# Performance work log

Hardware: AMD Instinct MI355X
Metric: run time of the kernel (lower is better)

The kernel has to match this reference:

```python
import jax, jax.numpy as jnp
import numpy as np

DIM = 1024
HEADS = 16
DIM_HEAD = DIM // HEADS  # 64
B, N = 4, 1024


def setup_inputs() -> dict:
    key = jax.random.key(0)
    ks = jax.random.split(key, 8)
    s = 1.0 / np.sqrt(DIM)
    inp = {
        "x": jax.random.normal(ks[0], (B, N, DIM), dtype=jnp.float32),
        # weights stored as [in, out] so y = x @ W (+ b), equivalent to torch Linear
        "Wq": jax.random.normal(ks[1], (DIM, DIM), dtype=jnp.float32) * s,
        "Wk": jax.random.normal(ks[2], (DIM, DIM), dtype=jnp.float32) * s,
        "Wv": jax.random.normal(ks[3], (DIM, DIM), dtype=jnp.float32) * s,
        "Wproj": jax.random.normal(ks[4], (DIM, DIM), dtype=jnp.float32) * s,
        "bproj": jnp.zeros((DIM,), dtype=jnp.float32),
        "Wpre": jax.random.normal(ks[5], (DIM, DIM), dtype=jnp.float32) * s,
        "bpre": jnp.zeros((DIM,), dtype=jnp.float32),
        # original init is -inf (non-runnable); use a finite trained value
        "pi": jnp.full((1,), 0.5, dtype=jnp.float32),
    }
    return inp


def reference(x, Wq, Wk, Wv, Wproj, bproj, Wpre, bpre, pi):
    b, n, c = x.shape
    h, dh = HEADS, DIM_HEAD
    residual = x
    # bias-logit path: Linear -> SiLU -> bmm with itself (dropout p=0 is identity)
    pre = jax.nn.silu(x @ Wpre + bpre)                       # [B,N,C]
    logits = jnp.einsum('bnc,bmc->bnm', pre, pre) / jnp.sqrt(jnp.float32(c))
    # QKV (x2 defaults to x)
    q = (x @ Wq).reshape(b, n, h, dh).transpose(0, 2, 1, 3)  # [B,H,N,Dh]
    k = (x @ Wk).reshape(b, n, h, dh).transpose(0, 2, 1, 3)
    v = (x @ Wv).reshape(b, n, h, dh).transpose(0, 2, 1, 3)
    score = jnp.einsum('bhnd,bhmd->bhnm', q, k) / jnp.sqrt(jnp.float32(dh))
    final_logits = pi[0] * logits[:, None, :, :] + score     # broadcast bias over heads
    attn = jax.nn.softmax(final_logits, axis=-1)
    out = jnp.einsum('bhnm,bhmd->bhnd', attn, v)             # [B,H,N,Dh]
    out = out.transpose(0, 2, 1, 3).reshape(b, n, h * dh)
    out = out @ Wproj + bproj
    return out + residual
```

## Files before the change

kernel.cpp:

```cpp
#include <hip/hip_runtime.h>

using bf16x8 = __attribute__((ext_vector_type(8))) short;
using v8bf   = __attribute__((ext_vector_type(8))) __bf16;
using f32x4  = __attribute__((ext_vector_type(4))) float;
using u32x2  = __attribute__((ext_vector_type(2))) unsigned;
using bf16x2 = __attribute__((ext_vector_type(2))) __bf16;

typedef const __attribute__((address_space(1))) void GASV;
typedef __attribute__((address_space(3))) void LASV;

template <typename V>
__device__ __forceinline__ auto mfma_bf16_impl(V a, V b, f32x4 c, int)
    -> decltype(__builtin_amdgcn_mfma_f32_16x16x32_bf16(a, b, c, 0, 0, 0)) {
  return __builtin_amdgcn_mfma_f32_16x16x32_bf16(a, b, c, 0, 0, 0);
}
template <typename V>
__device__ __forceinline__ f32x4 mfma_bf16_impl(V a, V b, f32x4 c, long) {
  return __builtin_amdgcn_mfma_f32_16x16x32_bf16(
      __builtin_bit_cast(v8bf, a), __builtin_bit_cast(v8bf, b), c, 0, 0, 0);
}
__device__ __forceinline__ f32x4 MFMA(bf16x8 a, bf16x8 b, f32x4 c) {
  return mfma_bf16_impl(a, b, c, 0);
}

__device__ __forceinline__ void async_lds16(const void* g, void* l) {
  __builtin_amdgcn_global_load_lds((GASV*)g, (LASV*)l, 16, 0, 0);
}

__device__ __forceinline__ unsigned short f2bf(float x) {
  unsigned u = __float_as_uint(x);
  u = u + 0x7fffu + ((u >> 16) & 1u);
  return (unsigned short)(u >> 16);
}

__device__ __forceinline__ unsigned pack_bf2(float lo, float hi) {
  bf16x2 t;
  t[0] = (__bf16)lo;
  t[1] = (__bf16)hi;
  return __builtin_bit_cast(unsigned, t);
}

#define LOG2E 1.4426950408889634f
#define SOFT_OFF 14.0f

__global__ __launch_bounds__(256) void k_prep(
    const float4* __restrict__ x, ushort4* __restrict__ xb,
    const float* __restrict__ w0, const float* __restrict__ w1,
    const float* __restrict__ w2, const float* __restrict__ w3,
    const float* __restrict__ w4, unsigned short* __restrict__ out) {
  const int bid = blockIdx.x, tid = threadIdx.x;
  if (bid < 4096) {
    const int i = bid * 256 + tid;
    float4 v = x[i];
    ushort4 p;
    p.x = f2bf(v.x); p.y = f2bf(v.y); p.z = f2bf(v.z); p.w = f2bf(v.w);
    xb[i] = p;
    return;
  }
  __shared__ float t[32][33];
  const int tb = bid - 4096;
  const int z = tb >> 10;
  const float* W = (z == 0) ? w0 : (z == 1) ? w1 : (z == 2) ? w2 : (z == 3) ? w3 : w4;
  const float sc = (z == 1) ? (LOG2E / 8.0f) : 1.0f;
  unsigned short* o = out + (size_t)z * (1u << 20);
  const int bx = (tb & 31) * 32, by = ((tb >> 5) & 31) * 32;
  const int tx = tid & 31, ty = tid >> 5;
#pragma unroll
  for (int i = 0; i < 4; ++i)
    t[ty + i * 8][tx] = W[(size_t)(by + ty + i * 8) * 1024 + bx + tx];
  __syncthreads();
#pragma unroll
  for (int i = 0; i < 4; ++i)
    o[(size_t)(bx + ty + i * 8) * 1024 + by + tx] = f2bf(t[tx][ty + i * 8] * sc);
}

template <int MI, int NI>
__device__ __forceinline__ void gemm_core_t(const unsigned short* __restrict__ A,
                                            const unsigned short* __restrict__ Bt,
                                            unsigned short* ldsA,
                                            unsigned short* ldsB,
                                            f32x4 acc[MI][NI]) {
  const int tid = threadIdx.x;
  const int w = tid >> 6, lane = tid & 63;
  const int lane15 = lane & 15, quad = lane >> 4;
  const int wm = w >> 1, wn = w & 1;
  for (int ko = 0; ko < 16; ++ko) {
    __syncthreads();
#pragma unroll
    for (int i = 0; i < MI; ++i) {
      const int p = i * 256 + tid;
      const int r = p >> 3, cc = (p & 7) ^ (r & 7);
      async_lds16(A + r * 1024 + ko * 64 + cc * 8, ldsA + (i * 256 + w * 64) * 8);
    }
#pragma unroll
    for (int i = 0; i < NI; ++i) {
      const int p = i * 256 + tid;
      const int r = p >> 3, cc = (p & 7) ^ (r & 7);
      async_lds16(Bt + r * 1024 + ko * 64 + cc * 8, ldsB + (i * 256 + w * 64) * 8);
    }
    __syncthreads();
    bf16x8 af[MI][2], bfr[NI][2];
#pragma unroll
    for (int t = 0; t < MI; ++t) {
      const int row = wm * (MI * 16) + t * 16 + lane15;
#pragma unroll
      for (int h = 0; h < 2; ++h)
        af[t][h] = *(const bf16x8*)&ldsA[row * 64 + (((h * 4 + quad) ^ (row & 7)) << 3)];
    }
#pragma unroll
    for (int t = 0; t < NI; ++t) {
      const int row = wn * (NI * 16) + t * 16 + lane15;
#pragma unroll
      for (int h = 0; h < 2; ++h)
        bfr[t][h] = *(const bf16x8*)&ldsB[row * 64 + (((h * 4 + quad) ^ (row & 7)) << 3)];
    }
#pragma unroll
    for (int mi = 0; mi < MI; ++mi)
#pragma unroll
      for (int ni = 0; ni < NI; ++ni) {
        acc[mi][ni] = MFMA(af[mi][0], bfr[ni][0], acc[mi][ni]);
        acc[mi][ni] = MFMA(af[mi][1], bfr[ni][1], acc[mi][ni]);
      }
  }
}

#define GEMM_PROLOGUE(MI_, NI_)                                      \
  __shared__ unsigned short ldsA[(MI_)*32 * 64];                     \
  __shared__ unsigned short ldsB[(NI_)*32 * 64];                     \
  f32x4 acc[MI_][NI_];                                               \
  {                                                                  \
    f32x4 z_ = {0.f, 0.f, 0.f, 0.f};                                 \
    for (int i_ = 0; i_ < (MI_); ++i_)                               \
      for (int j_ = 0; j_ < (NI_); ++j_) acc[i_][j_] = z_;           \
  }

#define GEMM_EPI_IDX(MI_, NI_)                                       \
  const int tid = threadIdx.x, w = tid >> 6, lane = tid & 63;        \
  const int lane15 = lane & 15, quad = lane >> 4;                    \
  const int wm = w >> 1, wn = w & 1;                                 \
  const int r0 = tm + wm * ((MI_)*16) + quad * 4;                    \
  const int c0 = tn + wn * ((NI_)*16) + lane15;

__global__ __launch_bounds__(512, 4) void k_gemm_qkvpre(
    const unsigned short* __restrict__ xb, const unsigned short* __restrict__ wt,
    const float* __restrict__ bpre, unsigned short* __restrict__ pre,
    unsigned short* __restrict__ qb, unsigned short* __restrict__ kb,
    unsigned short* __restrict__ vt) {
  __shared__ unsigned short ldsA[2][256 * 32];
  __shared__ unsigned short ldsB[2][128 * 32];
  const int bid = blockIdx.x;
  const int xcd = bid & 7, idx = bid >> 3;
  const int z = xcd >> 1, half = xcd & 1;
  int tm, tn;
  if (z == 3) {
    tm = half * 2048 + (idx >> 3) * 256;
    tn = (idx & 7) * 128;
  } else {
    tm = (idx >> 4) * 256;
    tn = half * 2048 + (idx & 15) * 128;
  }
  const unsigned short* At =
      (z == 3) ? xb + (size_t)tm * 1024
               : wt + (size_t)z * (1u << 20) + (size_t)tm * 1024;
  const unsigned short* Bt_ =
      (z == 3) ? wt + (size_t)3 * (1u << 20) + (size_t)tn * 1024
               : xb + (size_t)tn * 1024;

  const int tid = threadIdx.x, w = tid >> 6, lane = tid & 63;
  const int lane15 = lane & 15, quad = lane >> 4;
  const int wm = w >> 1, wn = w & 1;

  f32x4 acc[4][4];
  {
    f32x4 z_ = {0.f, 0.f, 0.f, 0.f};
#pragma unroll
    for (int i = 0; i < 4; ++i)
#pragma unroll
      for (int j = 0; j < 4; ++j) acc[i][j] = z_;
  }

  auto stage = [&](int ko, int buf) {
#pragma unroll
    for (int j = 0; j < 2; ++j) {
      const int p = j * 512 + tid;
      const int r = p >> 2, cc = (p & 3) ^ ((r >> 1) & 3);
      async_lds16(At + (size_t)r * 1024 + ko * 32 + cc * 8,
                  &ldsA[buf][(j * 512 + w * 64) * 8]);
    }
    {
      const int p = tid;
      const int r = p >> 2, cc = (p & 3) ^ ((r >> 1) & 3);
      async_lds16(Bt_ + (size_t)r * 1024 + ko * 32 + cc * 8,
                  &ldsB[buf][(w * 64) * 8]);
    }
  };

  stage(0, 0);
  __syncthreads();
  for (int t = 0; t < 32; ++t) {
    const int buf = t & 1;
    if (t + 1 < 32) stage(t + 1, buf ^ 1);
    const unsigned short* sA = ldsA[buf];
    const unsigned short* sB = ldsB[buf];
    bf16x8 af[4], bf[4];
#pragma unroll
    for (int mi = 0; mi < 4; ++mi) {
      const int row = wm * 64 + mi * 16 + lane15;
      af[mi] = *(const bf16x8*)&sA[row * 32 + ((quad ^ ((row >> 1) & 3)) << 3)];
    }
#pragma unroll
    for (int ni = 0; ni < 4; ++ni) {
      const int row = wn * 64 + ni * 16 + lane15;
      bf[ni] = *(const bf16x8*)&sB[row * 32 + ((quad ^ ((row >> 1) & 3)) << 3)];
    }
    __builtin_amdgcn_s_setprio(1);
#pragma unroll
    for (int mi = 0; mi < 4; ++mi)
#pragma unroll
      for (int ni = 0; ni < 4; ++ni)
        acc[mi][ni] = MFMA(af[mi], bf[ni], acc[mi][ni]);
    __builtin_amdgcn_s_setprio(0);
    __syncthreads();
  }

  const int r0 = tm + wm * 64 + quad * 4;
  const int c0 = tn + wn * 64 + lane15;
  if (z == 0) {
#pragma unroll
    for (int mf = 0; mf < 4; ++mf) {
      const float4 b4 = *(const float4*)&bpre[r0 + mf * 16];
#pragma unroll
      for (int nf = 0; nf < 4; ++nf) {
        const int seq = c0 + nf * 16;
        float vv[4];
#pragma unroll
        for (int rr = 0; rr < 4; ++rr) {
          float v = acc[mf][nf][rr] + ((const float*)&b4)[rr];
          vv[rr] = v / (1.0f + __expf(-v));
        }
        ushort4 pk;
        pk.x = f2bf(vv[0]); pk.y = f2bf(vv[1]);
        pk.z = f2bf(vv[2]); pk.w = f2bf(vv[3]);
        *(ushort4*)&pre[(size_t)seq * 1024 + r0 + mf * 16] = pk;
      }
    }
  } else if (z == 1 || z == 2) {
    unsigned short* dst = (z == 1) ? qb : kb;
#pragma unroll
    for (int mf = 0; mf < 4; ++mf)
#pragma unroll
      for (int nf = 0; nf < 4; ++nf) {
        const int seq = c0 + nf * 16;
        ushort4 pk;
        pk.x = f2bf(acc[mf][nf][0]); pk.y = f2bf(acc[mf][nf][1]);
        pk.z = f2bf(acc[mf][nf][2]); pk.w = f2bf(acc[mf][nf][3]);
        *(ushort4*)&dst[(size_t)seq * 1024 + r0 + mf * 16] = pk;
      }
  } else {
#pragma unroll
    for (int mf = 0; mf < 4; ++mf) {
      const int m = r0 + mf * 16;
      const int bb_ = m >> 10, nseq = m & 1023;
#pragma unroll
      for (int nf = 0; nf < 4; ++nf) {
        const int cg = c0 + nf * 16;
        const int hh = cg >> 6, dd = cg & 63;
        ushort4 pk;
        pk.x = f2bf(acc[mf][nf][0]); pk.y = f2bf(acc[mf][nf][1]);
        pk.z = f2bf(acc[mf][nf][2]); pk.w = f2bf(acc[mf][nf][3]);
        *(ushort4*)&vt[(size_t)(((bb_ * 16 + hh) << 6) + dd) * 1024 + nseq] = pk;
      }
    }
  }
}

__global__ __launch_bounds__(256) void k_gemm_logits(
    const unsigned short* __restrict__ pre, const float* __restrict__ pi,
    unsigned short* __restrict__ lg) {
  const int bz = blockIdx.z;
  const unsigned short* base = pre + ((size_t)bz << 20);
  const int tm = blockIdx.y * 64, tn = blockIdx.x * 128;
  GEMM_PROLOGUE(2, 4);
  gemm_core_t<2, 4>(base + (size_t)tm * 1024, base + (size_t)tn * 1024, ldsA, ldsB, acc);
  const float sc = pi[0] * (LOG2E / 32.0f);
  GEMM_EPI_IDX(2, 4);
#pragma unroll
  for (int mi = 0; mi < 2; ++mi)
#pragma unroll
    for (int ni = 0; ni < 4; ++ni) {
      const int col = c0 + ni * 16;
      ushort4 pk;
      pk.x = f2bf(acc[mi][ni][0] * sc); pk.y = f2bf(acc[mi][ni][1] * sc);
      pk.z = f2bf(acc[mi][ni][2] * sc); pk.w = f2bf(acc[mi][ni][3] * sc);
      *(ushort4*)&lg[((size_t)bz << 20) + (size_t)col * 1024 + r0 + mi * 16] = pk;
    }
}

__global__ __launch_bounds__(256) void k_gemm_out(
    const unsigned short* __restrict__ ao, const unsigned short* __restrict__ wtp,
    const float* __restrict__ bproj, const float* __restrict__ xres,
    float* __restrict__ out) {
  const int tm = blockIdx.x * 64, tn = blockIdx.y * 128;
  GEMM_PROLOGUE(2, 4);
  gemm_core_t<2, 4>(wtp + (size_t)tm * 1024, ao + (size_t)tn * 1024, ldsA, ldsB, acc);
  GEMM_EPI_IDX(2, 4);
#pragma unroll
  for (int mi = 0; mi < 2; ++mi) {
    const float4 b4 = *(const float4*)&bproj[r0 + mi * 16];
#pragma unroll
    for (int ni = 0; ni < 4; ++ni) {
      const int seq = c0 + ni * 16;
      const size_t idx = (size_t)seq * 1024 + r0 + mi * 16;
      const float4 rv = *(const float4*)&xres[idx];
      float4 ov;
      ov.x = acc[mi][ni][0] + b4.x + rv.x;
      ov.y = acc[mi][ni][1] + b4.y + rv.y;
      ov.z = acc[mi][ni][2] + b4.z + rv.z;
      ov.w = acc[mi][ni][3] + b4.w + rv.w;
      *(float4*)&out[idx] = ov;
    }
  }
}

__global__ __launch_bounds__(256, 2) void k_attn(
    const unsigned short* __restrict__ qb, const unsigned short* __restrict__ kb,
    const unsigned short* __restrict__ vt, const unsigned short* __restrict__ lg,
    unsigned short* __restrict__ ao) {
  __shared__ unsigned short ldsK[2 * 64 * 64];
  __shared__ unsigned short ldsV[2 * 64 * 64];
  const int bid = blockIdx.x;
  const int xcd = bid & 7, idx = bid >> 3;
  const int b = xcd >> 1, hg = xcd & 1;
  const int h = hg * 8 + (idx >> 3);
  const int q0 = (idx & 7) * 128;
  const int tid = threadIdx.x, w = tid >> 6, lane = tid & 63;
  const int lane15 = lane & 15, quad = lane >> 4;
  const int qw = q0 + w * 32;

  bf16x8 qf[2][2];
#pragma unroll
  for (int qh = 0; qh < 2; ++qh) {
    const unsigned short* qrow =
        qb + (size_t)((b << 10) + qw + qh * 16 + lane15) * 1024 + (h << 6);
    qf[qh][0] = *(const bf16x8*)(qrow + quad * 8);
    qf[qh][1] = *(const bf16x8*)(qrow + 32 + quad * 8);
  }
  const unsigned short* kbase = kb + ((size_t)(b << 10)) * 1024 + (h << 6);
  const unsigned short* vbase = vt + ((size_t)((b * 16 + h) << 6)) * 1024;
  const unsigned short* lgrow =
      lg + ((size_t)b << 20) + (size_t)(qw + lane15) * 1024 +
      (quad >> 1) * 16 + (quad & 1) * 4;

  float lcol[2] = {0.f, 0.f};
  f32x4 o[2][4];
  {
    f32x4 z_ = {0.f, 0.f, 0.f, 0.f};
#pragma unroll
    for (int qh = 0; qh < 2; ++qh)
#pragma unroll
      for (int nt = 0; nt < 4; ++nt) o[qh][nt] = z_;
  }

  uint2 lgc[2][4], lgn[2][4];

  auto stage = [&](int ch, unsigned short* sK, unsigned short* sV) {
    const int kv0 = ch * 64;
#pragma unroll
    for (int i = 0; i < 2; ++i) {
      const int p = i * 256 + tid;
      const int r = p >> 3, cc = (p & 7) ^ (r & 7);
      const int rk = (r & 0x27) | ((r & 8) << 1) | ((r & 16) >> 1);
      async_lds16(kbase + (size_t)(kv0 + rk) * 1024 + cc * 8,
                  sK + (i * 256 + w * 64) * 8);
      async_lds16(vbase + (size_t)r * 1024 + kv0 + cc * 8,
                  sV + (i * 256 + w * 64) * 8);
    }
  };
  auto lgload = [&](int ch, uint2 dst[2][4]) {
#pragma unroll
    for (int qh = 0; qh < 2; ++qh)
#pragma unroll
      for (int mi = 0; mi < 4; ++mi)
        dst[qh][mi] = *(const uint2*)(lgrow + qh * 16 * 1024 + ch * 64 +
                                      (mi >> 1) * 32 + (mi & 1) * 8);
  };
  auto compute = [&](const unsigned short* sK, const unsigned short* sV) {
    f32x4 s[2][4];
    __builtin_amdgcn_s_setprio(1);
#pragma unroll
    for (int mi = 0; mi < 4; ++mi) {
      const int row = mi * 16 + lane15;
      bf16x8 k0 = *(const bf16x8*)&sK[row * 64 + ((quad ^ (row & 7)) << 3)];
      bf16x8 k1 = *(const bf16x8*)&sK[row * 64 + (((4 + quad) ^ (row & 7)) << 3)];
#pragma unroll
      for (int qh = 0; qh < 2; ++qh) {
        f32x4 t;
        t[0] = __uint_as_float(lgc[qh][mi].x << 16);
        t[1] = __uint_as_float(lgc[qh][mi].x & 0xffff0000u);
        t[2] = __uint_as_float(lgc[qh][mi].y << 16);
        t[3] = __uint_as_float(lgc[qh][mi].y & 0xffff0000u);
        t = MFMA(k0, qf[qh][0], t);
        t = MFMA(k1, qf[qh][1], t);
        s[qh][mi] = t;
      }
    }
    __builtin_amdgcn_s_setprio(0);
    uint2 pk[2][4];
#pragma unroll
    for (int qh = 0; qh < 2; ++qh) {
      float rs = 0.f;
#pragma unroll
      for (int mi = 0; mi < 4; ++mi) {
        const float p0 = __builtin_amdgcn_exp2f(s[qh][mi][0] - SOFT_OFF);
        const float p1 = __builtin_amdgcn_exp2f(s[qh][mi][1] - SOFT_OFF);
        const float p2 = __builtin_amdgcn_exp2f(s[qh][mi][2] - SOFT_OFF);
        const float p3 = __builtin_amdgcn_exp2f(s[qh][mi][3] - SOFT_OFF);
        rs += (p0 + p1) + (p2 + p3);
        pk[qh][mi].x = pack_bf2(p0, p1);
        pk[qh][mi].y = pack_bf2(p2, p3);
      }
      lcol[qh] += rs;
    }

#pragma unroll
    for (int kp = 0; kp < 2; ++kp) {
      bf16x8 vf[4];
#pragma unroll
      for (int dt = 0; dt < 4; ++dt) {
        const int d = dt * 16 + lane15;
        vf[dt] = *(const bf16x8*)&sV[d * 64 +
                                     (((kp * 4 + quad) ^ (d & 7)) << 3)];
      }
#pragma unroll
      for (int qh = 0; qh < 2; ++qh) {
        u32x2 rx = __builtin_amdgcn_permlane16_swap(pk[qh][2 * kp].x,
                                                    pk[qh][2 * kp + 1].x, 0, 0);
        u32x2 ry = __builtin_amdgcn_permlane16_swap(pk[qh][2 * kp].y,
                                                    pk[qh][2 * kp + 1].y, 0, 0);
        uint4 bfv;
        bfv.x = rx.x;
        bfv.y = ry.x;
        bfv.z = rx.y;
        bfv.w = ry.y;
        const bf16x8 pf = __builtin_bit_cast(bf16x8, bfv);
        __builtin_amdgcn_s_setprio(1);
#pragma unroll
        for (int dt = 0; dt < 4; ++dt)
          o[qh][dt] = MFMA(vf[dt], pf, o[qh][dt]);
        __builtin_amdgcn_s_setprio(0);
      }
    }
  };

  unsigned short* sK0 = ldsK;
  unsigned short* sK1 = ldsK + 64 * 64;
  unsigned short* sV0 = ldsV;
  unsigned short* sV1 = ldsV + 64 * 64;

  stage(0, sK0, sV0);
  lgload(0, lgc);
  __syncthreads();

  for (int c = 0; c < 16; c += 2) {
    stage(c + 1, sK1, sV1);
    lgload(c + 1, lgn);
    compute(sK0, sV0);
    __syncthreads();
#pragma unroll
    for (int qh = 0; qh < 2; ++qh)
#pragma unroll
      for (int mi = 0; mi < 4; ++mi) lgc[qh][mi] = lgn[qh][mi];
    if (c + 2 < 16) {
      stage(c + 2, sK0, sV0);
      lgload(c + 2, lgn);
    }
    compute(sK1, sV1);
    __syncthreads();
#pragma unroll
    for (int qh = 0; qh < 2; ++qh)
#pragma unroll
      for (int mi = 0; mi < 4; ++mi) lgc[qh][mi] = lgn[qh][mi];
  }

#pragma unroll
  for (int qh = 0; qh < 2; ++qh) {
    float lc = lcol[qh];
    lc += __shfl_xor(lc, 16);
    lc += __shfl_xor(lc, 32);
    const float rinv = 1.0f / lc;
    const int m = (b << 10) + qw + qh * 16 + lane15;
#pragma unroll
    for (int dt = 0; dt < 4; ++dt) {
      ushort4 pkk;
      pkk.x = f2bf(o[qh][dt][0] * rinv);
      pkk.y = f2bf(o[qh][dt][1] * rinv);
      pkk.z = f2bf(o[qh][dt][2] * rinv);
      pkk.w = f2bf(o[qh][dt][3] * rinv);
      *(ushort4*)&ao[(size_t)m * 1024 + (h << 6) + dt * 16 + quad * 4] = pkk;
    }
  }
}

extern "C" void kernel_launch(void* const* d_in, const int* in_sizes, int n_in,
                              void* d_out, int out_size, void* d_ws, size_t ws_size,
                              hipStream_t stream) {
  const float* x     = (const float*)d_in[0];
  const float* Wq    = (const float*)d_in[1];
  const float* Wk    = (const float*)d_in[2];
  const float* Wv    = (const float*)d_in[3];
  const float* Wproj = (const float*)d_in[4];
  const float* bproj = (const float*)d_in[5];
  const float* Wpre  = (const float*)d_in[6];
  const float* bpre  = (const float*)d_in[7];
  const float* pi    = (const float*)d_in[8];
  float* out = (float*)d_out;
  char* ws = (char*)d_ws;

  unsigned short* xb  = (unsigned short*)(ws);
  unsigned short* wt  = (unsigned short*)(ws + (8u << 20));
  unsigned short* pre = (unsigned short*)(ws + (18u << 20));
  unsigned short* qb  = (unsigned short*)(ws + (26u << 20));
  unsigned short* kb  = (unsigned short*)(ws + (34u << 20));
  unsigned short* vt  = (unsigned short*)(ws + (42u << 20));
  unsigned short* lg  = xb;
  unsigned short* ao  = pre;

  k_prep<<<dim3(4096 + 5120), dim3(256), 0, stream>>>(
      (const float4*)x, (ushort4*)xb, Wpre, Wq, Wk, Wv, Wproj, wt);
  k_gemm_qkvpre<<<dim3(512), dim3(512), 0, stream>>>(xb, wt, bpre, pre, qb, kb, vt);
  k_gemm_logits<<<dim3(8, 16, 4), dim3(256), 0, stream>>>(pre, pi, lg);
  k_attn<<<dim3(512), dim3(256), 0, stream>>>(qb, kb, vt, lg, ao);
  k_gemm_out<<<dim3(16, 32, 1), dim3(256), 0, stream>>>(ao, wt + 4 * (1u << 20), bproj, x, out);
}
```

Before: 209.2 us.

## Load A operand fragments directly from global into registers, staging only B in LDS

The QKV/pre GEMM kernel no longer stages the 256-row A tile through LDS. Each wave now loads its own A fragments straight from global memory into registers, double-buffered across iterations, and only the B tile goes through async LDS copies. This removes the A-side LDS traffic and halves LDS footprint, which could allow more resident blocks. In exchange, A rows are read from global by both column-waves (wn=0/1) without sharing, the 16-byte loads per lane are strided by rows, and extra registers are used for two fragment sets.

```diff
diff --git a/kernel.cpp b/kernel.cpp
--- a/kernel.cpp
+++ b/kernel.cpp
@@ -146,7 +146,6 @@
     const float* __restrict__ bpre, unsigned short* __restrict__ pre,
     unsigned short* __restrict__ qb, unsigned short* __restrict__ kb,
     unsigned short* __restrict__ vt) {
-  __shared__ unsigned short ldsA[2][256 * 32];
   __shared__ unsigned short ldsB[2][128 * 32];
   const int bid = blockIdx.x;
   const int xcd = bid & 7, idx = bid >> 3;
@@ -179,35 +178,19 @@
       for (int j = 0; j < 4; ++j) acc[i][j] = z_;
   }
 
-  auto stage = [&](int ko, int buf) {
-#pragma unroll
-    for (int j = 0; j < 2; ++j) {
-      const int p = j * 512 + tid;
-      const int r = p >> 2, cc = (p & 3) ^ ((r >> 1) & 3);
-      async_lds16(At + (size_t)r * 1024 + ko * 32 + cc * 8,
-                  &ldsA[buf][(j * 512 + w * 64) * 8]);
-    }
-    {
-      const int p = tid;
-      const int r = p >> 2, cc = (p & 3) ^ ((r >> 1) & 3);
-      async_lds16(Bt_ + (size_t)r * 1024 + ko * 32 + cc * 8,
-                  &ldsB[buf][(w * 64) * 8]);
-    }
+  auto stageB = [&](int ko, int buf) {
+    const int r = tid >> 2, cc = (tid & 3) ^ ((r >> 1) & 3);
+    async_lds16(Bt_ + (size_t)r * 1024 + ko * 32 + cc * 8,
+                &ldsB[buf][(w * 64) * 8]);
   };
-
-  stage(0, 0);
-  __syncthreads();
-  for (int t = 0; t < 32; ++t) {
-    const int buf = t & 1;
-    if (t + 1 < 32) stage(t + 1, buf ^ 1);
-    const unsigned short* sA = ldsA[buf];
-    const unsigned short* sB = ldsB[buf];
-    bf16x8 af[4], bf[4];
-#pragma unroll
-    for (int mi = 0; mi < 4; ++mi) {
-      const int row = wm * 64 + mi * 16 + lane15;
-      af[mi] = *(const bf16x8*)&sA[row * 32 + ((quad ^ ((row >> 1) & 3)) << 3)];
-    }
+  const unsigned short* arow = At + (size_t)(wm * 64 + lane15) * 1024 + quad * 8;
+  auto loadA = [&](bf16x8 af[4], int ko) {
+#pragma unroll
+    for (int mi = 0; mi < 4; ++mi)
+      af[mi] = *(const bf16x8*)(arow + (size_t)(mi * 16) * 1024 + ko * 32);
+  };
+  auto step = [&](const unsigned short* sB, const bf16x8 af[4]) {
+    bf16x8 bf[4];
 #pragma unroll
     for (int ni = 0; ni < 4; ++ni) {
       const int row = wn * 64 + ni * 16 + lane15;
@@ -220,6 +203,18 @@
       for (int ni = 0; ni < 4; ++ni)
         acc[mi][ni] = MFMA(af[mi], bf[ni], acc[mi][ni]);
     __builtin_amdgcn_s_setprio(0);
+  };
+
+  bf16x8 afA[4], afB[4];
+  stageB(0, 0);
+  loadA(afA, 0);
+  __syncthreads();
+  for (int t = 0; t < 32; t += 2) {
+    if (t + 1 < 32) { stageB(t + 1, 1); loadA(afB, t + 1); }
+    step(ldsB[0], afA);
+    __syncthreads();
+    if (t + 2 < 32) { stageB(t + 2, 0); loadA(afA, t + 2); }
+    step(ldsB[1], afB);
     __syncthreads();
   }
 
```

After: 247.9 us. 1.19x slower.

## Double-buffer LDS in logits and output-projection GEMMs with K=32 stages

Applied to the files above, without the earlier changes.

Replaces the single-buffered K=64 GEMM core used by the logits and output-projection kernels with a double-buffered core that prefetches the next K=32 slice into the alternate LDS buffer while MFMAs run on the current one. This leaves one barrier per iteration instead of two and raises wave priority around the MFMA block. The swizzle is adapted to 32-wide rows and launch bounds request two blocks per CU. In exchange the loop runs twice as many iterations, each with fewer MFMAs to hide the load latency.

```diff
diff --git a/kernel.cpp b/kernel.cpp
--- a/kernel.cpp
+++ b/kernel.cpp
@@ -74,72 +74,55 @@
     o[(size_t)(bx + ty + i * 8) * 1024 + by + tx] = f2bf(t[tx][ty + i * 8] * sc);
 }
 
-template <int MI, int NI>
-__device__ __forceinline__ void gemm_core_t(const unsigned short* __restrict__ A,
-                                            const unsigned short* __restrict__ Bt,
-                                            unsigned short* ldsA,
-                                            unsigned short* ldsB,
-                                            f32x4 acc[MI][NI]) {
-  const int tid = threadIdx.x;
-  const int w = tid >> 6, lane = tid & 63;
+__device__ __forceinline__ void gemm64x128_core(
+    const unsigned short* __restrict__ At, const unsigned short* __restrict__ Bt,
+    unsigned short (*ldsA)[64 * 32], unsigned short (*ldsB)[128 * 32],
+    f32x4 acc[2][4]) {
+  const int tid = threadIdx.x, w = tid >> 6, lane = tid & 63;
   const int lane15 = lane & 15, quad = lane >> 4;
   const int wm = w >> 1, wn = w & 1;
-  for (int ko = 0; ko < 16; ++ko) {
+  auto stage = [&](int ko, int buf) {
+    {
+      const int r = tid >> 2, cc = (tid & 3) ^ ((r >> 1) & 3);
+      async_lds16(At + (size_t)r * 1024 + ko * 32 + cc * 8,
+                  &ldsA[buf][(w * 64) * 8]);
+    }
+#pragma unroll
+    for (int j = 0; j < 2; ++j) {
+      const int p = j * 256 + tid;
+      const int r = p >> 2, cc = (p & 3) ^ ((r >> 1) & 3);
+      async_lds16(Bt + (size_t)r * 1024 + ko * 32 + cc * 8,
+                  &ldsB[buf][(j * 256 + w * 64) * 8]);
+    }
+  };
+  stage(0, 0);
+  __syncthreads();
+  for (int t = 0; t < 32; ++t) {
+    const int buf = t & 1;
+    if (t + 1 < 32) stage(t + 1, buf ^ 1);
+    const unsigned short* sA = ldsA[buf];
+    const unsigned short* sB = ldsB[buf];
+    bf16x8 af[2], bf[4];
+#pragma unroll
+    for (int mi = 0; mi < 2; ++mi) {
+      const int row = wm * 32 + mi * 16 + lane15;
+      af[mi] = *(const bf16x8*)&sA[row * 32 + ((quad ^ ((row >> 1) & 3)) << 3)];
+    }
+#pragma unroll
+    for (int ni = 0; ni < 4; ++ni) {
+      const int row = wn * 64 + ni * 16 + lane15;
+      bf[ni] = *(const bf16x8*)&sB[row * 32 + ((quad ^ ((row >> 1) & 3)) << 3)];
+    }
+    __builtin_amdgcn_s_setprio(1);
+#pragma unroll
+    for (int mi = 0; mi < 2; ++mi)
+#pragma unroll
+      for (int ni = 0; ni < 4; ++ni)
+        acc[mi][ni] = MFMA(af[mi], bf[ni], acc[mi][ni]);
+    __builtin_amdgcn_s_setprio(0);
     __syncthreads();
-#pragma unroll
-    for (int i = 0; i < MI; ++i) {
-      const int p = i * 256 + tid;
-      const int r = p >> 3, cc = (p & 7) ^ (r & 7);
-      async_lds16(A + r * 1024 + ko * 64 + cc * 8, ldsA + (i * 256 + w * 64) * 8);
-    }
-#pragma unroll
-    for (int i = 0; i < NI; ++i) {
-      const int p = i * 256 + tid;
-      const int r = p >> 3, cc = (p & 7) ^ (r & 7);
-      async_lds16(Bt + r * 1024 + ko * 64 + cc * 8, ldsB + (i * 256 + w * 64) * 8);
-    }
-    __syncthreads();
-    bf16x8 af[MI][2], bfr[NI][2];
-#pragma unroll
-    for (int t = 0; t < MI; ++t) {
-      const int row = wm * (MI * 16) + t * 16 + lane15;
-#pragma unroll
-      for (int h = 0; h < 2; ++h)
-        af[t][h] = *(const bf16x8*)&ldsA[row * 64 + (((h * 4 + quad) ^ (row & 7)) << 3)];
-    }
-#pragma unroll
-    for (int t = 0; t < NI; ++t) {
-      const int row = wn * (NI * 16) + t * 16 + lane15;
-#pragma unroll
-      for (int h = 0; h < 2; ++h)
-        bfr[t][h] = *(const bf16x8*)&ldsB[row * 64 + (((h * 4 + quad) ^ (row & 7)) << 3)];
-    }
-#pragma unroll
-    for (int mi = 0; mi < MI; ++mi)
-#pragma unroll
-      for (int ni = 0; ni < NI; ++ni) {
-        acc[mi][ni] = MFMA(af[mi][0], bfr[ni][0], acc[mi][ni]);
-        acc[mi][ni] = MFMA(af[mi][1], bfr[ni][1], acc[mi][ni]);
-      }
-  }
-}
-
-#define GEMM_PROLOGUE(MI_, NI_)                                      \
-  __shared__ unsigned short ldsA[(MI_)*32 * 64];                     \
-  __shared__ unsigned short ldsB[(NI_)*32 * 64];                     \
-  f32x4 acc[MI_][NI_];                                               \
-  {                                                                  \
-    f32x4 z_ = {0.f, 0.f, 0.f, 0.f};                                 \
-    for (int i_ = 0; i_ < (MI_); ++i_)                               \
-      for (int j_ = 0; j_ < (NI_); ++j_) acc[i_][j_] = z_;           \
-  }
-
-#define GEMM_EPI_IDX(MI_, NI_)                                       \
-  const int tid = threadIdx.x, w = tid >> 6, lane = tid & 63;        \
-  const int lane15 = lane & 15, quad = lane >> 4;                    \
-  const int wm = w >> 1, wn = w & 1;                                 \
-  const int r0 = tm + wm * ((MI_)*16) + quad * 4;                    \
-  const int c0 = tn + wn * ((NI_)*16) + lane15;
+  }
+}
 
 __global__ __launch_bounds__(512, 4) void k_gemm_qkvpre(
     const unsigned short* __restrict__ xb, const unsigned short* __restrict__ wt,
@@ -274,16 +257,30 @@
   }
 }
 
-__global__ __launch_bounds__(256) void k_gemm_logits(
+__global__ __launch_bounds__(256, 2) void k_gemm_logits(
     const unsigned short* __restrict__ pre, const float* __restrict__ pi,
     unsigned short* __restrict__ lg) {
+  __shared__ unsigned short ldsA[2][64 * 32];
+  __shared__ unsigned short ldsB[2][128 * 32];
   const int bz = blockIdx.z;
   const unsigned short* base = pre + ((size_t)bz << 20);
   const int tm = blockIdx.y * 64, tn = blockIdx.x * 128;
-  GEMM_PROLOGUE(2, 4);
-  gemm_core_t<2, 4>(base + (size_t)tm * 1024, base + (size_t)tn * 1024, ldsA, ldsB, acc);
+  f32x4 acc[2][4];
+  {
+    f32x4 z_ = {0.f, 0.f, 0.f, 0.f};
+#pragma unroll
+    for (int i = 0; i < 2; ++i)
+#pragma unroll
+      for (int j = 0; j < 4; ++j) acc[i][j] = z_;
+  }
+  gemm64x128_core(base + (size_t)tm * 1024, base + (size_t)tn * 1024,
+                  ldsA, ldsB, acc);
   const float sc = pi[0] * (LOG2E / 32.0f);
-  GEMM_EPI_IDX(2, 4);
+  const int tid = threadIdx.x, w = tid >> 6, lane = tid & 63;
+  const int lane15 = lane & 15, quad = lane >> 4;
+  const int wm = w >> 1, wn = w & 1;
+  const int r0 = tm + wm * 32 + quad * 4;
+  const int c0 = tn + wn * 64 + lane15;
 #pragma unroll
   for (int mi = 0; mi < 2; ++mi)
 #pragma unroll
@@ -296,14 +293,28 @@
     }
 }
 
-__global__ __launch_bounds__(256) void k_gemm_out(
+__global__ __launch_bounds__(256, 2) void k_gemm_out(
     const unsigned short* __restrict__ ao, const unsigned short* __restrict__ wtp,
     const float* __restrict__ bproj, const float* __restrict__ xres,
     float* __restrict__ out) {
+  __shared__ unsigned short ldsA[2][64 * 32];
+  __shared__ unsigned short ldsB[2][128 * 32];
   const int tm = blockIdx.x * 64, tn = blockIdx.y * 128;
-  GEMM_PROLOGUE(2, 4);
-  gemm_core_t<2, 4>(wtp + (size_t)tm * 1024, ao + (size_t)tn * 1024, ldsA, ldsB, acc);
-  GEMM_EPI_IDX(2, 4);
+  f32x4 acc[2][4];
+  {
+    f32x4 z_ = {0.f, 0.f, 0.f, 0.f};
+#pragma unroll
+    for (int i = 0; i < 2; ++i)
+#pragma unroll
+      for (int j = 0; j < 4; ++j) acc[i][j] = z_;
+  }
+  gemm64x128_core(wtp + (size_t)tm * 1024, ao + (size_t)tn * 1024,
+                  ldsA, ldsB, acc);
+  const int tid = threadIdx.x, w = tid >> 6, lane = tid & 63;
+  const int lane15 = lane & 15, quad = lane >> 4;
+  const int wm = w >> 1, wn = w & 1;
+  const int r0 = tm + wm * 32 + quad * 4;
+  const int c0 = tn + wn * 64 + lane15;
 #pragma unroll
   for (int mi = 0; mi < 2; ++mi) {
     const float4 b4 = *(const float4*)&bproj[r0 + mi * 16];
```

Result: slower. 217.1 us (+3.8%).
